# Optimization experiments

Hardware: AMD Instinct MI355X
Metric: run time of the kernel (lower is better)

Reference implementation:

```python
import jax, jax.numpy as jnp
import numpy as np

NODES_PER_GRAPH = 40
NEG_SLOPE = 0.1


def gcn_conv(x, src, dst, deg_inv_sqrt, W, b):
    # PyG GCNConv: h = x @ W.T; symmetric-normalized aggregation with self-loops; + bias
    h = x @ W.T                                   # [N, out]
    norm = deg_inv_sqrt[src] * deg_inv_sqrt[dst]  # [E]
    msgs = h[src] * norm[:, None]                 # [E, out]
    agg = jax.ops.segment_sum(msgs, dst, num_segments=x.shape[0])
    # self-loop contribution: norm_ii = deg_inv_sqrt[i]^2 = 1/deg[i]
    agg = agg + h * (deg_inv_sqrt ** 2)[:, None]
    return agg + b


def setup_inputs() -> dict:
    key = jax.random.key(0)
    ks = jax.random.split(key, 12)
    N, E, C = 200000, 1000000, 40
    hid1, hid2, hid3, lin1, lin2, out = 128, 256, 128, 512, 128, 1

    def glorot(k, shape):
        fan_in = shape[-1]
        return jax.random.normal(k, shape, dtype=jnp.float32) * (1.0 / np.sqrt(fan_in))

    x = jax.random.normal(ks[0], (N, C), dtype=jnp.float32)
    edge_index = jax.random.randint(ks[1], (2, E), 0, N, dtype=jnp.int64)
    return {
        "x": x,
        "edge_index": edge_index,
        "W1": glorot(ks[2], (hid1, C)), "b1": jnp.zeros((hid1,), jnp.float32),
        "W2": glorot(ks[3], (hid2, hid1)), "b2": jnp.zeros((hid2,), jnp.float32),
        "W3": glorot(ks[4], (hid3, hid2)), "b3": jnp.zeros((hid3,), jnp.float32),
        "L1w": glorot(ks[5], (lin1, NODES_PER_GRAPH * hid3)), "L1b": jnp.zeros((lin1,), jnp.float32),
        "L2w": glorot(ks[6], (lin2, lin1)), "L2b": jnp.zeros((lin2,), jnp.float32),
        "L3w": glorot(ks[7], (out, lin2)), "L3b": jnp.zeros((out,), jnp.float32),
    }


def reference(x, edge_index, W1, b1, W2, b2, W3, b3, L1w, L1b, L2w, L2b, L3w, L3b):
    N = x.shape[0]
    src, dst = edge_index[0], edge_index[1]
    # degree with self-loops (edge weight 1), shared by all three convs
    deg = jax.ops.segment_sum(jnp.ones_like(dst, dtype=x.dtype), dst, num_segments=N) + 1.0
    deg_inv_sqrt = jax.lax.rsqrt(deg)

    lrelu = lambda v: jax.nn.leaky_relu(v, NEG_SLOPE)

    h = lrelu(gcn_conv(x, src, dst, deg_inv_sqrt, W1, b1))
    # dropout is identity in eval mode
    h = lrelu(gcn_conv(h, src, dst, deg_inv_sqrt, W2, b2))
    h = lrelu(gcn_conv(h, src, dst, deg_inv_sqrt, W3, b3))

    g = h.reshape(N // NODES_PER_GRAPH, -1)   # [G, 40*hid3]
    g = lrelu(g @ L1w.T + L1b)
    g = lrelu(g @ L2w.T + L2b)
    g = g @ L3w.T + L3b
    return jax.nn.sigmoid(g)                   # [G, 1]
```

## Files before the change

### kernel.cpp

```cpp
#include <hip/hip_runtime.h>
#include <cmath>

#define CDIV(a,b) (((a)+(b)-1)/(b))

typedef unsigned short bf16_t;
using short8 = __attribute__((ext_vector_type(8))) short;
using f32x4  = __attribute__((ext_vector_type(4))) float;
using u16x4  = __attribute__((ext_vector_type(4))) unsigned short;
using u16x8  = __attribute__((ext_vector_type(8))) unsigned short;

__device__ __forceinline__ float bf2f(unsigned short b) {
    unsigned u = ((unsigned)b) << 16;
    float f;
    __builtin_memcpy(&f, &u, 4);
    return f;
}
__device__ __forceinline__ unsigned short f2bf(float f) {
    unsigned u;
    __builtin_memcpy(&u, &f, 4);
    u = (u + 0x7FFFu + ((u >> 16) & 1u)) >> 16;
    return (unsigned short)u;
}

__device__ __forceinline__ void gload16(const bf16_t* g, unsigned short* l) {
    __builtin_amdgcn_global_load_lds(
        (const __attribute__((address_space(1))) void*)(g),
        (__attribute__((address_space(3))) void*)(l), 16, 0, 0);
}

__global__ void k_detect(const int* __restrict__ ei, int* __restrict__ flag) {
    int t = threadIdx.x;
    unsigned v = (unsigned)ei[2 * t + 1];
    unsigned long long m = __ballot(v != 0u);
    if (t == 0) *flag = (m == 0ULL) ? 1 : 0;
}

__device__ __forceinline__ int edge_src(const int* ei, int E, int f, int i) {
    return f ? ei[2 * (size_t)i] : ei[i];
}
__device__ __forceinline__ int edge_dst(const int* ei, int E, int f, int i) {
    return f ? ei[2 * ((size_t)E + (size_t)i)] : ei[(size_t)E + (size_t)i];
}

__global__ __launch_bounds__(256) void k_packhist(const int* __restrict__ ei, int E,
                                                  const int* __restrict__ flag,
                                                  int* __restrict__ src32,
                                                  int* __restrict__ dst32,
                                                  int* __restrict__ cnt8, int N) {
    int i = blockIdx.x * 256 + threadIdx.x;
    if (i >= E) return;
    int f = *flag;
    int s = edge_src(ei, E, f, i);
    int d = edge_dst(ei, E, f, i);
    src32[i] = s;
    dst32[i] = d;
    if ((unsigned)d < (unsigned)N)
        atomicAdd(&cnt8[(blockIdx.x & 7) * N + d], 1);
}

__global__ void k_blockred(const int* __restrict__ cnt8, int* __restrict__ bsum, int N) {
    __shared__ int sd[256];
    int b = blockIdx.x, t = threadIdx.x;
    int base = b * 1024 + t * 4;
    int s = 0;
#pragma unroll
    for (int i = 0; i < 4; i++) {
        int idx = base + i;
        if (idx < N)
#pragma unroll
            for (int r = 0; r < 8; r++) s += cnt8[r * N + idx];
    }
    sd[t] = s; __syncthreads();
    for (int off = 128; off > 0; off >>= 1) { if (t < off) sd[t] += sd[t + off]; __syncthreads(); }
    if (t == 0) bsum[b] = sd[0];
}

__global__ void k_scanwrite(const int* __restrict__ cnt8, const int* __restrict__ bsum,
                            int* __restrict__ rowptr, int* __restrict__ cur,
                            float* __restrict__ dis, int N, int nb) {
    __shared__ int sb[256];
    __shared__ int sd[256];
    int b = blockIdx.x, t = threadIdx.x;
    int v0 = (t < nb) ? bsum[t] : 0;
    sb[t] = v0; __syncthreads();
    for (int off = 1; off < 256; off <<= 1) {
        int y = (t >= off) ? sb[t - off] : 0;
        __syncthreads();
        sb[t] += y;
        __syncthreads();
    }
    int block_pre = (b == 0) ? 0 : sb[b - 1];

    int base = b * 1024 + t * 4;
    int tot[4]; int s = 0;
#pragma unroll
    for (int i = 0; i < 4; i++) {
        int idx = base + i;
        tot[i] = 0;
        if (idx < N) {
#pragma unroll
            for (int r = 0; r < 8; r++) tot[i] += cnt8[r * N + idx];
        }
        s += tot[i];
    }
    sd[t] = s; __syncthreads();
    for (int off = 1; off < 256; off <<= 1) {
        int y = (t >= off) ? sd[t - off] : 0;
        __syncthreads();
        sd[t] += y;
        __syncthreads();
    }
    int pre = block_pre + sd[t] - s;
#pragma unroll
    for (int i = 0; i < 4; i++) {
        int idx = base + i;
        if (idx < N) {
            rowptr[idx] = pre;
            cur[idx] = pre;
            dis[idx] = rsqrtf((float)tot[i] + 1.0f);
            pre += tot[i];
        } else if (idx == N) {
            rowptr[N] = pre;
        }
    }
}

#define FILL_EPB 4096
__global__ __launch_bounds__(256) void k_fill_r(
        const int* __restrict__ src32, const int* __restrict__ dst32, int E,
        int* __restrict__ cur, int* __restrict__ csr, int N, int NR) {
    int r = blockIdx.x & 7;
    int chunk = blockIdx.x >> 3;
    int lo = r * NR;
    int hi = min(lo + NR, N);
    int base = chunk * FILL_EPB;
    int end = min(base + FILL_EPB, E);
    for (int i = base + threadIdx.x; i < end; i += 256) {
        int d = dst32[i];
        if (d >= lo && d < hi) {
            int s = src32[i];
            if ((unsigned)s < (unsigned)N) {
                int p = atomicAdd(&cur[d], 1);
                csr[p] = s;
            }
        }
    }
}


struct WcSeg { const float* src; bf16_t* dst; int M, KW, KP, nchunk; };

__global__ __launch_bounds__(256) void k_wconv(WcSeg s0, WcSeg s1, WcSeg s2,
                                               WcSeg s3, WcSeg s4, WcSeg s5,
                                               int total) {
    int i = blockIdx.x * 256 + threadIdx.x;
    if (i >= total) return;
    WcSeg s;
    if (i < s0.nchunk) s = s0;
    else if ((i -= s0.nchunk) < s1.nchunk) s = s1;
    else if ((i -= s1.nchunk) < s2.nchunk) s = s2;
    else if ((i -= s2.nchunk) < s3.nchunk) s = s3;
    else if ((i -= s3.nchunk) < s4.nchunk) s = s4;
    else { i -= s4.nchunk; s = s5; }
    int cpr = s.KP >> 3;
    int row = i / cpr, kk = (i % cpr) << 3;
    short8 v = {};
    if (kk < s.KW) {
        const float4* p = (const float4*)(s.src + (size_t)row * s.KW + kk);
        float4 a = p[0], b = p[1];
        v[0] = (short)f2bf(a.x); v[1] = (short)f2bf(a.y);
        v[2] = (short)f2bf(a.z); v[3] = (short)f2bf(a.w);
        v[4] = (short)f2bf(b.x); v[5] = (short)f2bf(b.y);
        v[6] = (short)f2bf(b.z); v[7] = (short)f2bf(b.w);
    }
    *(short8*)(s.dst + (size_t)row * s.KP + kk) = v;
}


template <bool CBF, bool BIAS, int ACT, bool SPLIT>
__global__ __launch_bounds__(256) void gemm_mfma(
        const bf16_t* __restrict__ A, const bf16_t* __restrict__ Wb,
        const float* __restrict__ bias, void* __restrict__ Cv,
        int N, int K, int M, int Kseg, int nx, int ny) {
    constexpr int BM = 128, BK = 64;
    __shared__ __align__(16) unsigned short lds[4 * 64 * 68];
    unsigned short* Als = lds;
    unsigned short* Bls = lds + BM * BK;

    int t = threadIdx.x;
    int lane = t & 63, wid = t >> 6;
    int quad = lane >> 4, l15 = lane & 15;
    int wave_m = wid & 1, wave_n = wid >> 1;

    int bx, by, bz;
    if (SPLIT) {
        int bid = (int)blockIdx.x;
        int xcd = bid & 7, li = bid >> 3;
        bx = li % nx;
        int pl = li / nx;
        int ppx = (int)(gridDim.x >> 3) / nx;
        int pair = xcd * ppx + pl;
        by = pair % ny;
        bz = pair / ny;
    } else {
        bx = blockIdx.x; by = blockIdx.y; bz = 0;
    }

    int bm0 = by * BM;
    int bn0 = bx * BM;
    int kbeg = SPLIT ? bz * Kseg : 0;
    int kend = SPLIT ? min(kbeg + Kseg, K) : K;

    f32x4 acc[4][4] = {};

    for (int k0 = kbeg; k0 < kend; k0 += BK) {
#pragma unroll
        for (int it = 0; it < 4; it++) {
            int idx = t + it * 256;
            int row = idx >> 3, sc = idx & 7;
            int c = sc ^ (row & 7);
            int ga = bm0 + row; if (ga >= N) ga = N - 1;
            gload16(A + (size_t)ga * K + k0 + c * 8, Als + idx * 8);
            gload16(Wb + (size_t)(bn0 + row) * K + k0 + c * 8, Bls + idx * 8);
        }
        __syncthreads();

#pragma unroll
        for (int ks = 0; ks < 2; ks++) {
            short8 af[4], bfr[4];
            int ck = ks * 4 + quad;
            int sw = (ck ^ (l15 & 7)) << 3;
#pragma unroll
            for (int mt = 0; mt < 4; mt++)
                af[mt] = *(const short8*)&Als[(wave_m * 64 + mt * 16 + l15) * BK + sw];
#pragma unroll
            for (int nt = 0; nt < 4; nt++)
                bfr[nt] = *(const short8*)&Bls[(wave_n * 64 + nt * 16 + l15) * BK + sw];
#pragma unroll
            for (int mt = 0; mt < 4; mt++)
#pragma unroll
                for (int nt = 0; nt < 4; nt++)
                    acc[mt][nt] = __builtin_amdgcn_mfma_f32_16x16x32_bf16(
                        af[mt], bfr[nt], acc[mt][nt], 0, 0, 0);
        }
        __syncthreads();
    }

    if (!SPLIT && CBF) {
        constexpr int TST = 68;
        unsigned short* tw = lds + wid * 64 * TST;
#pragma unroll
        for (int mt = 0; mt < 4; mt++) {
#pragma unroll
            for (int nt = 0; nt < 4; nt++) {
                int tcol = nt * 16 + l15;
                float bv = BIAS ? bias[bn0 + wave_n * 64 + tcol] : 0.f;
#pragma unroll
                for (int r = 0; r < 4; r++) {
                    float x = acc[mt][nt][r];
                    if (BIAS) x += bv;
                    if (ACT == 1) x = x > 0.f ? x : 0.1f * x;
                    tw[(mt * 16 + quad * 4 + r) * TST + tcol] = f2bf(x);
                }
            }
        }
        __syncthreads();
        bf16_t* C = (bf16_t*)Cv;
        int lrow0 = lane >> 3, lcol = (lane & 7) * 8;
#pragma unroll
        for (int it = 0; it < 8; it++) {
            int lrow = it * 8 + lrow0;
            int row = bm0 + wave_m * 64 + lrow;
            if (row < N) {
                u16x8 v = *(const u16x8*)&tw[lrow * TST + lcol];
                *(u16x8*)&C[(size_t)row * M + bn0 + wave_n * 64 + lcol] = v;
            }
        }
    } else {
        float* Pz = SPLIT ? ((float*)Cv + (size_t)bz * N * M) : (float*)Cv;
#pragma unroll
        for (int mt = 0; mt < 4; mt++) {
            int rbase = bm0 + wave_m * 64 + mt * 16 + quad * 4;
#pragma unroll
            for (int nt = 0; nt < 4; nt++) {
                int col = bn0 + wave_n * 64 + nt * 16 + l15;
                float bv = (BIAS && !SPLIT) ? bias[col] : 0.f;
#pragma unroll
                for (int r = 0; r < 4; r++) {
                    int row = rbase + r;
                    if (row >= N) continue;
                    float x = acc[mt][nt][r];
                    if (!SPLIT) {
                        if (BIAS) x += bv;
                        if (ACT == 1) x = x > 0.f ? x : 0.1f * x;
                    }
                    Pz[(size_t)row * M + col] = x;
                }
            }
        }
    }
}

__global__ __launch_bounds__(256, 3) void gemm_fused23(
        const bf16_t* __restrict__ A,
        const bf16_t* __restrict__ W2,
        const float*  __restrict__ b2,
        const bf16_t* __restrict__ W3,
        bf16_t* __restrict__ C,
        int N) {
    __shared__ __align__(16) unsigned short lds[24576];
    unsigned short* Als  = lds;
    unsigned short* Bls  = lds + 4096;
    unsigned short* H2ls = lds;
    unsigned short* B2ls = lds + 16384;

    int t = threadIdx.x;
    int lane = t & 63, wid = t >> 6;
    int quad = lane >> 4, l15 = lane & 15;
    int wm = wid & 1, wn = wid >> 1;
    int bm0 = blockIdx.x * 64;

    float bv[8];
#pragma unroll
    for (int nt = 0; nt < 8; nt++) bv[nt] = b2[wn * 128 + nt * 16 + l15];

    f32x4 acc1[2][8] = {};
    for (int k0 = 0; k0 < 128; k0 += 64) {
#pragma unroll
        for (int it = 0; it < 2; it++) {
            int idx = t + it * 256;
            int row = idx >> 3, sc = idx & 7;
            int c = sc ^ (row & 7);
            int g = bm0 + row; if (g >= N) g = N - 1;
            gload16(A + (size_t)g * 128 + k0 + c * 8, Als + idx * 8);
        }
#pragma unroll
        for (int it = 0; it < 8; it++) {
            int idx = t + it * 256;
            int row = idx >> 3, sc = idx & 7;
            int c = sc ^ (row & 7);
            gload16(W2 + (size_t)row * 128 + k0 + c * 8, Bls + idx * 8);
        }
        __syncthreads();
#pragma unroll
        for (int ks = 0; ks < 2; ks++) {
            int ck = ks * 4 + quad;
            int sw = (ck ^ (l15 & 7)) << 3;
            short8 af[2];
#pragma unroll
            for (int mt = 0; mt < 2; mt++)
                af[mt] = *(const short8*)&Als[(wm * 32 + mt * 16 + l15) * 64 + sw];
#pragma unroll
            for (int nt = 0; nt < 8; nt++) {
                short8 bfr = *(const short8*)&Bls[(wn * 128 + nt * 16 + l15) * 64 + sw];
#pragma unroll
                for (int mt = 0; mt < 2; mt++)
                    acc1[mt][nt] = __builtin_amdgcn_mfma_f32_16x16x32_bf16(
                        af[mt], bfr, acc1[mt][nt], 0, 0, 0);
            }
        }
        __syncthreads();
    }

#pragma unroll
    for (int it = 0; it < 4; it++) {
        int idx = t + it * 256;
        int row = idx >> 3, sc = idx & 7;
        int c = sc ^ (row & 7);
        gload16(W3 + (size_t)row * 256 + c * 8, B2ls + idx * 8);
    }

#pragma unroll
    for (int mt = 0; mt < 2; mt++) {
#pragma unroll
        for (int nt = 0; nt < 8; nt++) {
            int col = wn * 128 + nt * 16 + l15;
            int chunk = col >> 3, within = col & 7;
#pragma unroll
            for (int r = 0; r < 4; r++) {
                int row = wm * 32 + mt * 16 + quad * 4 + r;
                float xv = acc1[mt][nt][r] + bv[nt];
                xv = xv > 0.f ? xv : 0.1f * xv;
                H2ls[row * 256 + ((chunk ^ (row & 7)) << 3) + within] = f2bf(xv);
            }
        }
    }
    __syncthreads();

    f32x4 acc2[2][4] = {};
    for (int k0 = 0; k0 < 256; k0 += 64) {
        if (k0 > 0) {
#pragma unroll
            for (int it = 0; it < 4; it++) {
                int idx = t + it * 256;
                int row = idx >> 3, sc = idx & 7;
                int c = sc ^ (row & 7);
                gload16(W3 + (size_t)row * 256 + k0 + c * 8, B2ls + idx * 8);
            }
            __syncthreads();
        }
#pragma unroll
        for (int ks = 0; ks < 2; ks++) {
            int kc = (k0 >> 3) + ks * 4 + quad;
            int swa = (kc ^ (l15 & 7)) << 3;
            int swb = ((ks * 4 + quad) ^ (l15 & 7)) << 3;
            short8 af[2], bfr[4];
#pragma unroll
            for (int mt = 0; mt < 2; mt++)
                af[mt] = *(const short8*)&H2ls[(wm * 32 + mt * 16 + l15) * 256 + swa];
#pragma unroll
            for (int nt = 0; nt < 4; nt++)
                bfr[nt] = *(const short8*)&B2ls[(wn * 64 + nt * 16 + l15) * 64 + swb];
#pragma unroll
            for (int mt = 0; mt < 2; mt++)
#pragma unroll
                for (int nt = 0; nt < 4; nt++)
                    acc2[mt][nt] = __builtin_amdgcn_mfma_f32_16x16x32_bf16(
                        af[mt], bfr[nt], acc2[mt][nt], 0, 0, 0);
        }
        __syncthreads();
    }

    constexpr int TST = 68;
    unsigned short* tw = lds + wid * 32 * TST;
#pragma unroll
    for (int mt = 0; mt < 2; mt++) {
#pragma unroll
        for (int nt = 0; nt < 4; nt++) {
            int tcol = nt * 16 + l15;
#pragma unroll
            for (int r = 0; r < 4; r++)
                tw[(mt * 16 + quad * 4 + r) * TST + tcol] = f2bf(acc2[mt][nt][r]);
        }
    }
    __syncthreads();
    int lrow0 = lane >> 3, lcol = (lane & 7) * 8;
#pragma unroll
    for (int it = 0; it < 4; it++) {
        int lrow = it * 8 + lrow0;
        int row = bm0 + wm * 32 + lrow;
        if (row < N) {
            u16x8 v = *(const u16x8*)&tw[lrow * TST + lcol];
            *(u16x8*)&C[(size_t)row * 128 + wn * 64 + lcol] = v;
        }
    }
}


template <int S, bool CBF, int ACT>
__global__ __launch_bounds__(256) void k_red(
        const float* __restrict__ part, const float* __restrict__ bias,
        void* __restrict__ out, int GM, int Mmask) {
    int i = (blockIdx.x * 256 + threadIdx.x) * 4;
    if (i >= GM) return;
    float4 s = *(const float4*)&part[i];
#pragma unroll
    for (int z = 1; z < S; z++) {
        float4 p = *(const float4*)&part[(size_t)z * GM + i];
        s.x += p.x; s.y += p.y; s.z += p.z; s.w += p.w;
    }
    float4 b = *(const float4*)&bias[i & Mmask];
    float v[4] = {s.x + b.x, s.y + b.y, s.z + b.z, s.w + b.w};
#pragma unroll
    for (int j = 0; j < 4; j++)
        if (ACT == 1) v[j] = v[j] > 0.f ? v[j] : 0.1f * v[j];
    if (CBF) {
        u16x4 o = {f2bf(v[0]), f2bf(v[1]), f2bf(v[2]), f2bf(v[3])};
        *(u16x4*)((bf16_t*)out + i) = o;
    } else {
        float4 o; o.x = v[0]; o.y = v[1]; o.z = v[2]; o.w = v[3];
        *(float4*)((float*)out + i) = o;
    }
}


template <int F, bool BACT>
__global__ __launch_bounds__(256) void k_agg(
        const bf16_t* __restrict__ H, const int* __restrict__ rowptr,
        const int* __restrict__ csr, const float* __restrict__ dis,
        const float* __restrict__ bias, bf16_t* __restrict__ out, int N) {
    constexpr int SUB = F / 8;
    constexpr int NPW = 64 / SUB;
    constexpr int SH  = (SUB == 16) ? 4 : 3;
    int gtid = blockIdx.x * 256 + threadIdx.x;
    int wave = gtid >> 6, lane = gtid & 63;
    int sub = lane >> SH, sl = lane & (SUB - 1);
    int node = wave * NPW + sub;
    if (node >= N) return;
    float di = dis[node];
    int s = rowptr[node], e = rowptr[node + 1];

    auto load_row = [&](const bf16_t* p, float (&r)[8]) {
        u16x8 v = *(const u16x8*)p;
#pragma unroll
        for (int f = 0; f < 8; f++) r[f] = bf2f(v[f]);
    };

    float acc[8], acc2[8];
    {
        float r[8];
        load_row(H + (size_t)node * F + sl * 8, r);
        float sln = di * di;
#pragma unroll
        for (int f = 0; f < 8; f++) { acc[f] = r[f] * sln; acc2[f] = 0.f; }
    }
    int p = s;
    for (; p + 4 <= e; p += 4) {
        int s0 = csr[p], s1 = csr[p + 1], s2 = csr[p + 2], s3 = csr[p + 3];
        float n0 = dis[s0] * di, n1 = dis[s1] * di;
        float n2 = dis[s2] * di, n3 = dis[s3] * di;
        float r0[8], r1[8], r2[8], r3[8];
        load_row(H + (size_t)s0 * F + sl * 8, r0);
        load_row(H + (size_t)s1 * F + sl * 8, r1);
        load_row(H + (size_t)s2 * F + sl * 8, r2);
        load_row(H + (size_t)s3 * F + sl * 8, r3);
#pragma unroll
        for (int f = 0; f < 8; f++) {
            acc[f]  += r0[f] * n0; acc2[f] += r1[f] * n1;
            acc[f]  += r2[f] * n2; acc2[f] += r3[f] * n3;
        }
    }
    if (p + 2 <= e) {
        int s0 = csr[p], s1 = csr[p + 1];
        float n0 = dis[s0] * di, n1 = dis[s1] * di;
        float r0[8], r1[8];
        load_row(H + (size_t)s0 * F + sl * 8, r0);
        load_row(H + (size_t)s1 * F + sl * 8, r1);
#pragma unroll
        for (int f = 0; f < 8; f++) { acc[f] += r0[f] * n0; acc2[f] += r1[f] * n1; }
        p += 2;
    }
    if (p < e) {
        int s0 = csr[p];
        float n0 = dis[s0] * di;
        float r0[8];
        load_row(H + (size_t)s0 * F + sl * 8, r0);
#pragma unroll
        for (int f = 0; f < 8; f++) acc[f] += r0[f] * n0;
    }

    float o[8];
#pragma unroll
    for (int f = 0; f < 8; f++) {
        float v = acc[f] + acc2[f];
        if (BACT) {
            v += bias[sl * 8 + f];
            v = v > 0.f ? v : 0.1f * v;
        }
        o[f] = v;
    }
    u16x8 w = {f2bf(o[0]), f2bf(o[1]), f2bf(o[2]), f2bf(o[3]),
               f2bf(o[4]), f2bf(o[5]), f2bf(o[6]), f2bf(o[7])};
    *(u16x8*)(out + (size_t)node * F + sl * 8) = w;
}


__global__ __launch_bounds__(256) void k_head2(
        const float* __restrict__ part, const float* __restrict__ L2b,
        const float* __restrict__ L3w, const float* __restrict__ L3b,
        float* __restrict__ out, int G) {
    int wv = (int)((blockIdx.x * blockDim.x + threadIdx.x) >> 6);
    int lane = threadIdx.x & 63;
    if (wv >= G) return;
    size_t base = (size_t)wv * 128 + lane * 2;
    size_t GM = (size_t)G * 128;
    float2 s = *(const float2*)&part[base];
#pragma unroll
    for (int z = 1; z < 4; z++) {
        float2 p = *(const float2*)&part[z * GM + base];
        s.x += p.x; s.y += p.y;
    }
    float2 b = *(const float2*)&L2b[lane * 2];
    float vx = s.x + b.x, vy = s.y + b.y;
    vx = vx > 0.f ? vx : 0.1f * vx;
    vy = vy > 0.f ? vy : 0.1f * vy;
    float2 wl = *(const float2*)&L3w[lane * 2];
    float d = vx * wl.x + vy * wl.y;
    for (int off = 32; off > 0; off >>= 1) d += __shfl_xor(d, off, 64);
    if (lane == 0) out[wv] = 1.f / (1.f + expf(-(d + L3b[0])));
}


extern "C" void kernel_launch(void* const* d_in, const int* in_sizes, int n_in,
                              void* d_out, int out_size, void* d_ws, size_t ws_size,
                              hipStream_t stream) {
    const float* x   = (const float*)d_in[0];
    const int*   ei  = (const int*)d_in[1];
    const float* W1  = (const float*)d_in[2];  const float* b1  = (const float*)d_in[3];
    const float* W2  = (const float*)d_in[4];  const float* b2  = (const float*)d_in[5];
    const float* W3  = (const float*)d_in[6];  const float* b3  = (const float*)d_in[7];
    const float* L1w = (const float*)d_in[8];  const float* L1b = (const float*)d_in[9];
    const float* L2w = (const float*)d_in[10]; const float* L2b = (const float*)d_in[11];
    const float* L3w = (const float*)d_in[12]; const float* L3b = (const float*)d_in[13];
    float* out = (float*)d_out;

    const int C = 40;
    const int N = in_sizes[0] / C;
    const int E = in_sizes[1] / 2;
    const int G = N / 40;
    const int H1d = 128, H2d = 256, H3d = 128, M1 = 512, M2 = 128;
    const int K1 = 40 * H3d;

    char* wsb = (char*)d_ws;
    size_t off = 0;
    auto alloc = [&](size_t bytes) -> void* {
        void* p = wsb + off;
        off += (bytes + 255) & ~(size_t)255;
        return p;
    };
    int*    flag   = (int*)alloc(4);
    int*    cnt8   = (int*)alloc(4 * 8 * (size_t)N);
    int*    rowptr = (int*)alloc(4 * (size_t)(N + 1));
    int*    cur    = (int*)alloc(4 * (size_t)N);
    int*    csr    = (int*)alloc(4 * (size_t)E);
    int*    bsum   = (int*)alloc(4 * 512);
    float*  dis    = (float*)alloc(4 * (size_t)N);
    bf16_t* Hb     = (bf16_t*)alloc(2 * (size_t)N * H2d);
    bf16_t* Xb     = (bf16_t*)alloc(2 * (size_t)N * H2d);
    bf16_t* g1b    = (bf16_t*)alloc(2 * (size_t)G * M1);
    bf16_t* W1b    = (bf16_t*)alloc(2 * (size_t)H1d * 64);
    bf16_t* W2b    = (bf16_t*)alloc(2 * (size_t)H2d * H1d);
    bf16_t* W3b    = (bf16_t*)alloc(2 * (size_t)H3d * H2d);
    bf16_t* L1wb   = (bf16_t*)alloc(2 * (size_t)M1 * K1);
    bf16_t* L2wb   = (bf16_t*)alloc(2 * (size_t)M2 * M1);
    if (off > ws_size) return;

    int* src32 = (int*)Xb;
    int* dst32 = src32 + E;
    bf16_t* xb   = Hb;
    bf16_t* A1b  = Xb;
    bf16_t* H1   = Hb;
    bf16_t* A2   = Xb;
    bf16_t* H3p  = Xb;
    bf16_t* X3   = Hb;
    float*  part = (float*)Xb;

    WcSeg s0 = {W1,  W1b,  H1d, 40,  64,  H1d * 64 / 8};
    WcSeg s1 = {W2,  W2b,  H2d, H1d, H1d, H2d * H1d / 8};
    WcSeg s2 = {W3,  W3b,  H3d, H2d, H2d, H3d * H2d / 8};
    WcSeg s3 = {L1w, L1wb, M1,  K1,  K1,  M1 * K1 / 8};
    WcSeg s4 = {L2w, L2wb, M2,  M1,  M1,  M2 * M1 / 8};
    WcSeg s5 = {x,   xb,   N,   40,  64,  N * 64 / 8};
    int wtotal = s0.nchunk + s1.nchunk + s2.nchunk + s3.nchunk + s4.nchunk + s5.nchunk;
    k_wconv<<<CDIV(wtotal, 256), 256, 0, stream>>>(s0, s1, s2, s3, s4, s5, wtotal);

    hipMemsetAsync(cnt8, 0, sizeof(int) * 8 * (size_t)N, stream);
    k_detect<<<1, 64, 0, stream>>>(ei, flag);
    k_packhist<<<CDIV(E, 256), 256, 0, stream>>>(ei, E, flag, src32, dst32, cnt8, N);
    int nb = CDIV(N + 1, 1024);
    k_blockred<<<nb, 256, 0, stream>>>(cnt8, bsum, N);
    k_scanwrite<<<nb, 256, 0, stream>>>(cnt8, bsum, rowptr, cur, dis, N, nb);
    int NR = CDIV(N, 8);
    k_fill_r<<<8 * CDIV(E, FILL_EPB), 256, 0, stream>>>(src32, dst32, E, cur, csr, N, NR);

    const int NB = CDIV(N, 128);
    const int GB = CDIV(G, 128);

    k_agg<64, false><<<CDIV(N, 32), 256, 0, stream>>>(xb, rowptr, csr, dis, nullptr, A1b, N);
    gemm_mfma<true, true, 1, false><<<dim3(1, NB), 256, 0, stream>>>(A1b, W1b, b1, H1, N, 64, H1d, 0, 0, 0);
    k_agg<128, false><<<CDIV(N, 16), 256, 0, stream>>>(H1, rowptr, csr, dis, nullptr, A2, N);
    gemm_fused23<<<CDIV(N, 64), 256, 0, stream>>>(A2, W2b, b2, W3b, H3p, N);
    k_agg<128, true><<<CDIV(N, 16), 256, 0, stream>>>(H3p, rowptr, csr, dis, b3, X3, N);

    gemm_mfma<false, false, 0, true><<<960, 256, 0, stream>>>(X3, L1wb, nullptr, part, G, K1, M1, 896, 4, 40);
    k_red<6, true, 1><<<CDIV(G * M1 / 4, 256), 256, 0, stream>>>(part, L1b, g1b, G * M1, M1 - 1);
    gemm_mfma<false, false, 0, true><<<160, 256, 0, stream>>>(g1b, L2wb, nullptr, part, G, M1, M2, M1 / 4, 1, 40);
    k_head2<<<CDIV(G, 4), 256, 0, stream>>>(part, L2b, L3w, L3b, out, G);
}
```

Baseline: 483.8 us.

## Fuse split-K reduction into MLP layer-2 GEMM and merge small setup kernels

The split-K partial reduction, bias and leaky-ReLU of the first MLP layer move into a new layer-2 GEMM that reduces the six partials while loading its A tile, so the separate reduction kernel and its bf16 intermediate go away. The edge-format detection now runs inside the pack/histogram kernel, and the histogram counters are zeroed by extra threads in the weight-conversion kernel instead of a memset. This cuts launches and one intermediate round trip through memory. In exchange, each of the four K-slices rereads the six fp32 partials, and every block repeats the detection ballot.

```diff
diff --git a/kernel.cpp b/kernel.cpp
--- a/kernel.cpp
+++ b/kernel.cpp
@@ -28,13 +28,6 @@
         (__attribute__((address_space(3))) void*)(l), 16, 0, 0);
 }
 
-__global__ void k_detect(const int* __restrict__ ei, int* __restrict__ flag) {
-    int t = threadIdx.x;
-    unsigned v = (unsigned)ei[2 * t + 1];
-    unsigned long long m = __ballot(v != 0u);
-    if (t == 0) *flag = (m == 0ULL) ? 1 : 0;
-}
-
 __device__ __forceinline__ int edge_src(const int* ei, int E, int f, int i) {
     return f ? ei[2 * (size_t)i] : ei[i];
 }
@@ -43,13 +36,20 @@
 }
 
 __global__ __launch_bounds__(256) void k_packhist(const int* __restrict__ ei, int E,
-                                                  const int* __restrict__ flag,
                                                   int* __restrict__ src32,
                                                   int* __restrict__ dst32,
                                                   int* __restrict__ cnt8, int N) {
-    int i = blockIdx.x * 256 + threadIdx.x;
+    __shared__ int sflag;
+    int t = threadIdx.x;
+    if (t < 64) {
+        unsigned v = (unsigned)ei[2 * t + 1];
+        unsigned long long m = __ballot(v != 0u);
+        if (t == 0) sflag = (m == 0ULL) ? 1 : 0;
+    }
+    __syncthreads();
+    int i = blockIdx.x * 256 + t;
     if (i >= E) return;
-    int f = *flag;
+    int f = sflag;
     int s = edge_src(ei, E, f, i);
     int d = edge_dst(ei, E, f, i);
     src32[i] = s;
@@ -152,9 +152,15 @@
 
 __global__ __launch_bounds__(256) void k_wconv(WcSeg s0, WcSeg s1, WcSeg s2,
                                                WcSeg s3, WcSeg s4, WcSeg s5,
+                                               int wtotal, int* __restrict__ zdst,
                                                int total) {
     int i = blockIdx.x * 256 + threadIdx.x;
     if (i >= total) return;
+    if (i >= wtotal) {
+        int4 z = {0, 0, 0, 0};
+        *(int4*)(zdst + (size_t)(i - wtotal) * 4) = z;
+        return;
+    }
     WcSeg s;
     if (i < s0.nchunk) s = s0;
     else if ((i -= s0.nchunk) < s1.nchunk) s = s1;
@@ -301,6 +307,105 @@
     }
 }
 
+__global__ __launch_bounds__(256) void gemm_mlp2(
+        const float* __restrict__ part6,
+        const float* __restrict__ L1b,
+        const bf16_t* __restrict__ Wb,
+        float* __restrict__ Pout,
+        int G) {
+    constexpr int BM = 128, BK = 64, K = 512, M = 128, NY = 40;
+    __shared__ __align__(16) unsigned short lds[2 * BM * BK];
+    unsigned short* Als = lds;
+    unsigned short* Bls = lds + BM * BK;
+
+    int t = threadIdx.x;
+    int lane = t & 63, wid = t >> 6;
+    int quad = lane >> 4, l15 = lane & 15;
+    int wave_m = wid & 1, wave_n = wid >> 1;
+
+    int bid = (int)blockIdx.x;
+    int xcd = bid & 7, li = bid >> 3;
+    int ppx = (int)(gridDim.x >> 3);
+    int pair = xcd * ppx + li;
+    int by = pair % NY;
+    int bz = pair / NY;
+
+    int bm0 = by * BM;
+    int kbeg = bz * (K / 4);
+    size_t GK = (size_t)G * K;
+
+    f32x4 acc[4][4] = {};
+
+    for (int k0 = kbeg; k0 < kbeg + K / 4; k0 += BK) {
+#pragma unroll
+        for (int it = 0; it < 4; it++) {
+            int idx = t + it * 256;
+            int row = idx >> 3, sc = idx & 7;
+            int cW = sc ^ (row & 7);
+            gload16(Wb + (size_t)row * K + k0 + cW * 8, Bls + idx * 8);
+            int g = bm0 + row; if (g >= G) g = G - 1;
+            const float* pb = part6 + (size_t)g * K + k0 + sc * 8;
+            float v[8] = {};
+#pragma unroll
+            for (int z = 0; z < 6; z++) {
+                const float* pz = pb + (size_t)z * GK;
+                float4 a = *(const float4*)pz;
+                float4 b = *(const float4*)(pz + 4);
+                v[0] += a.x; v[1] += a.y; v[2] += a.z; v[3] += a.w;
+                v[4] += b.x; v[5] += b.y; v[6] += b.z; v[7] += b.w;
+            }
+            float4 b0 = *(const float4*)&L1b[k0 + sc * 8];
+            float4 b1 = *(const float4*)&L1b[k0 + sc * 8 + 4];
+            float bb[8] = {b0.x, b0.y, b0.z, b0.w, b1.x, b1.y, b1.z, b1.w};
+            u16x8 o;
+#pragma unroll
+            for (int j = 0; j < 8; j++) {
+                float xv = v[j] + bb[j];
+                xv = xv > 0.f ? xv : 0.1f * xv;
+                o[j] = f2bf(xv);
+            }
+            *(u16x8*)&Als[row * BK + ((sc ^ (row & 7)) << 3)] = o;
+        }
+        __syncthreads();
+
+#pragma unroll
+        for (int ks = 0; ks < 2; ks++) {
+            short8 af[4], bfr[4];
+            int ck = ks * 4 + quad;
+            int sw = (ck ^ (l15 & 7)) << 3;
+#pragma unroll
+            for (int mt = 0; mt < 4; mt++)
+                af[mt] = *(const short8*)&Als[(wave_m * 64 + mt * 16 + l15) * BK + sw];
+#pragma unroll
+            for (int nt = 0; nt < 4; nt++)
+                bfr[nt] = *(const short8*)&Bls[(wave_n * 64 + nt * 16 + l15) * BK + sw];
+#pragma unroll
+            for (int mt = 0; mt < 4; mt++)
+#pragma unroll
+                for (int nt = 0; nt < 4; nt++)
+                    acc[mt][nt] = __builtin_amdgcn_mfma_f32_16x16x32_bf16(
+                        af[mt], bfr[nt], acc[mt][nt], 0, 0, 0);
+        }
+        __syncthreads();
+    }
+
+    float* Pz = Pout + (size_t)bz * G * M;
+#pragma unroll
+    for (int mt = 0; mt < 4; mt++) {
+        int rbase = bm0 + wave_m * 64 + mt * 16 + quad * 4;
+#pragma unroll
+        for (int nt = 0; nt < 4; nt++) {
+            int col = wave_n * 64 + nt * 16 + l15;
+#pragma unroll
+            for (int r = 0; r < 4; r++) {
+                int row = rbase + r;
+                if (row >= G) continue;
+                Pz[(size_t)row * M + col] = acc[mt][nt][r];
+            }
+        }
+    }
+}
+
 __global__ __launch_bounds__(256, 3) void gemm_fused23(
         const bf16_t* __restrict__ A,
         const bf16_t* __restrict__ W2,
@@ -443,33 +548,6 @@
             u16x8 v = *(const u16x8*)&tw[lrow * TST + lcol];
             *(u16x8*)&C[(size_t)row * 128 + wn * 64 + lcol] = v;
         }
-    }
-}
-
-
-template <int S, bool CBF, int ACT>
-__global__ __launch_bounds__(256) void k_red(
-        const float* __restrict__ part, const float* __restrict__ bias,
-        void* __restrict__ out, int GM, int Mmask) {
-    int i = (blockIdx.x * 256 + threadIdx.x) * 4;
-    if (i >= GM) return;
-    float4 s = *(const float4*)&part[i];
-#pragma unroll
-    for (int z = 1; z < S; z++) {
-        float4 p = *(const float4*)&part[(size_t)z * GM + i];
-        s.x += p.x; s.y += p.y; s.z += p.z; s.w += p.w;
-    }
-    float4 b = *(const float4*)&bias[i & Mmask];
-    float v[4] = {s.x + b.x, s.y + b.y, s.z + b.z, s.w + b.w};
-#pragma unroll
-    for (int j = 0; j < 4; j++)
-        if (ACT == 1) v[j] = v[j] > 0.f ? v[j] : 0.1f * v[j];
-    if (CBF) {
-        u16x4 o = {f2bf(v[0]), f2bf(v[1]), f2bf(v[2]), f2bf(v[3])};
-        *(u16x4*)((bf16_t*)out + i) = o;
-    } else {
-        float4 o; o.x = v[0]; o.y = v[1]; o.z = v[2]; o.w = v[3];
-        *(float4*)((float*)out + i) = o;
     }
 }
 
@@ -608,7 +686,6 @@
         off += (bytes + 255) & ~(size_t)255;
         return p;
     };
-    int*    flag   = (int*)alloc(4);
     int*    cnt8   = (int*)alloc(4 * 8 * (size_t)N);
     int*    rowptr = (int*)alloc(4 * (size_t)(N + 1));
     int*    cur    = (int*)alloc(4 * (size_t)N);
@@ -617,7 +694,6 @@
     float*  dis    = (float*)alloc(4 * (size_t)N);
     bf16_t* Hb     = (bf16_t*)alloc(2 * (size_t)N * H2d);
     bf16_t* Xb     = (bf16_t*)alloc(2 * (size_t)N * H2d);
-    bf16_t* g1b    = (bf16_t*)alloc(2 * (size_t)G * M1);
     bf16_t* W1b    = (bf16_t*)alloc(2 * (size_t)H1d * 64);
     bf16_t* W2b    = (bf16_t*)alloc(2 * (size_t)H2d * H1d);
     bf16_t* W3b    = (bf16_t*)alloc(2 * (size_t)H3d * H2d);
@@ -634,6 +710,7 @@
     bf16_t* H3p  = Xb;
     bf16_t* X3   = Hb;
     float*  part = (float*)Xb;
+    float*  part2 = part + 6 * (size_t)G * M1;
 
     WcSeg s0 = {W1,  W1b,  H1d, 40,  64,  H1d * 64 / 8};
     WcSeg s1 = {W2,  W2b,  H2d, H1d, H1d, H2d * H1d / 8};
@@ -642,11 +719,11 @@
     WcSeg s4 = {L2w, L2wb, M2,  M1,  M1,  M2 * M1 / 8};
     WcSeg s5 = {x,   xb,   N,   40,  64,  N * 64 / 8};
     int wtotal = s0.nchunk + s1.nchunk + s2.nchunk + s3.nchunk + s4.nchunk + s5.nchunk;
-    k_wconv<<<CDIV(wtotal, 256), 256, 0, stream>>>(s0, s1, s2, s3, s4, s5, wtotal);
-
-    hipMemsetAsync(cnt8, 0, sizeof(int) * 8 * (size_t)N, stream);
-    k_detect<<<1, 64, 0, stream>>>(ei, flag);
-    k_packhist<<<CDIV(E, 256), 256, 0, stream>>>(ei, E, flag, src32, dst32, cnt8, N);
+    int ztotal = wtotal + 2 * N;
+    k_wconv<<<CDIV(ztotal, 256), 256, 0, stream>>>(s0, s1, s2, s3, s4, s5,
+                                                   wtotal, cnt8, ztotal);
+
+    k_packhist<<<CDIV(E, 256), 256, 0, stream>>>(ei, E, src32, dst32, cnt8, N);
     int nb = CDIV(N + 1, 1024);
     k_blockred<<<nb, 256, 0, stream>>>(cnt8, bsum, N);
     k_scanwrite<<<nb, 256, 0, stream>>>(cnt8, bsum, rowptr, cur, dis, N, nb);
@@ -663,7 +740,6 @@
     k_agg<128, true><<<CDIV(N, 16), 256, 0, stream>>>(H3p, rowptr, csr, dis, b3, X3, N);
 
     gemm_mfma<false, false, 0, true><<<960, 256, 0, stream>>>(X3, L1wb, nullptr, part, G, K1, M1, 896, 4, 40);
-    k_red<6, true, 1><<<CDIV(G * M1 / 4, 256), 256, 0, stream>>>(part, L1b, g1b, G * M1, M1 - 1);
-    gemm_mfma<false, false, 0, true><<<160, 256, 0, stream>>>(g1b, L2wb, nullptr, part, G, M1, M2, M1 / 4, 1, 40);
-    k_head2<<<CDIV(G, 4), 256, 0, stream>>>(part, L2b, L3w, L3b, out, G);
-}
+    gemm_mlp2<<<160, 256, 0, stream>>>(part, L1b, L2wb, part2, G);
+    k_head2<<<CDIV(G, 4), 256, 0, stream>>>(part2, L2b, L3w, L3b, out, G);
+}
```

Result: no change. 480.4 us (-0.7%).
